# Optimization experiments

Measured on AMD Instinct MI355X. Metric: run time of the kernel, lower is better.

## Reference

```python
import jax, jax.numpy as jnp
import numpy as np
from jax.scipy.linalg import expm

D_LOGIC = 128
D_MEM = 16
SO_DIM = D_MEM * (D_MEM - 1) // 2  # 120


def _linear_init(key, fan_in, shape):
    bound = 1.0 / np.sqrt(fan_in)
    return jax.random.uniform(key, shape, jnp.float32, -bound, bound)


def setup_inputs() -> dict:
    key = jax.random.key(0)
    ks = jax.random.split(key, 14)
    B, S = 4, 128
    return {
        "x_logic": jax.random.normal(ks[0], (B, S, D_LOGIC), jnp.float32),
        "x_memory": jax.random.normal(ks[1], (B, S, D_MEM), jnp.float32),
        # W_Q / W_K
        "Wq": _linear_init(ks[2], D_LOGIC, (D_LOGIC, D_LOGIC)),
        "bq": _linear_init(ks[3], D_LOGIC, (D_LOGIC,)),
        "Wk": _linear_init(ks[4], D_LOGIC, (D_LOGIC, D_LOGIC)),
        "bk": _linear_init(ks[5], D_LOGIC, (D_LOGIC,)),
        # gamma_net: Linear(d_logic, 2*d_logic) -> Tanh -> Linear(2*d_logic, so_dim)
        "W1": _linear_init(ks[6], D_LOGIC, (2 * D_LOGIC, D_LOGIC)),
        "b1": _linear_init(ks[7], D_LOGIC, (2 * D_LOGIC,)),
        "W2": _linear_init(ks[8], 2 * D_LOGIC, (SO_DIM, 2 * D_LOGIC)),
        "b2": _linear_init(ks[9], 2 * D_LOGIC, (SO_DIM,)),
        # out_proj: Linear(d_memory, d_memory)
        "Wo": _linear_init(ks[10], D_MEM, (D_MEM, D_MEM)),
        "bo": _linear_init(ks[11], D_MEM, (D_MEM,)),
    }


def reference(x_logic, x_memory, Wq, bq, Wk, bk, W1, b1, W2, b2, Wo, bo):
    B, S, d_logic = x_logic.shape
    dm = x_memory.shape[-1]

    # attention over logic stream
    Q = x_logic @ Wq.T + bq
    K = x_logic @ Wk.T + bk
    attn = jax.nn.softmax(
        jnp.einsum("bjd,bid->bji", Q, K) / jnp.sqrt(jnp.float32(d_logic)), axis=-1
    )  # [B, S(j), S(i)]

    # per-pair Lie-algebra params: delta[b,j,i] = x_logic[b,j] - x_logic[b,i]
    delta = x_logic[:, :, None, :] - x_logic[:, None, :, :]  # [B,S,S,d_logic]
    h = jnp.tanh(delta @ W1.T + b1)
    lie = h @ W2.T + b2  # [B,S,S,so_dim]

    # scatter into skew-symmetric matrices [B,S,S,dm,dm]
    r, c = np.triu_indices(dm, k=1)
    skew = jnp.zeros((B, S, S, dm, dm), x_logic.dtype)
    skew = skew.at[..., r, c].set(lie)
    skew = skew.at[..., c, r].set(-lie)

    # Lie-group exponential -> orthogonal transport matrices
    T_all = expm(skew)  # [B,S,S,dm,dm]

    # transported[b,j,i,:] = T[b,j,i] @ x_memory[b,i]
    transported = jnp.einsum("bjide,bie->bjid", T_all, x_memory)

    # attention-weighted aggregation over i
    settled = jnp.einsum("bji,bjid->bjd", attn, transported)  # [B,S,dm]

    out = settled @ Wo.T + bo
    return out, T_all
```

## Files before the change

kernel.cpp:

```cpp
#include <hip/hip_runtime.h>
#include <hip/hip_fp16.h>

#define S_LEN 128
#define DLOG  128
#define DMEM  16
#define SO    120
#define HDIM  256

typedef _Float16 v8h __attribute__((ext_vector_type(8)));
typedef __fp16 v2hf __attribute__((ext_vector_type(2)));
typedef float v4f __attribute__((ext_vector_type(4)));

union PkU { v2hf h; unsigned u; };
union V8U { v8h v; int u[4]; };

__device__ __forceinline__ v8h splat8(float x) {
  _Float16 h = (_Float16)x;
  v8h v = {h, h, h, h, h, h, h, h};
  return v;
}

__global__ __launch_bounds__(512) void qku_kernel(
    const float* __restrict__ xl, const float* __restrict__ Wq,
    const float* __restrict__ bq, const float* __restrict__ Wk,
    const float* __restrict__ bk, const float* __restrict__ W1,
    float* __restrict__ Q, float* __restrict__ K, float* __restrict__ u) {
  int bj = blockIdx.x, t = threadIdx.x;
  int lane = t & 63, wu = t >> 6;
  int half = lane >> 5, l5 = lane & 31;
  float4 xv = *(const float4*)(xl + bj * 128 + 4 * l5);
  int seg = wu >> 1;
  const float* wb;
  if (seg == 0) wb = Wq;
  else if (seg == 1) wb = Wk - 128 * 128;
  else wb = W1 - 256 * 128;
  #pragma unroll 4
  for (int step = 0; step < 32; ++step) {
    int ro = wu * 64 + 2 * step + half;
    float4 wv = *(const float4*)(wb + ro * 128 + 4 * l5);
    float v = fmaf(wv.x, xv.x, fmaf(wv.y, xv.y, fmaf(wv.z, xv.z, wv.w * xv.w)));
    v += __shfl_xor(v, 1, 64);
    v += __shfl_xor(v, 2, 64);
    v += __shfl_xor(v, 4, 64);
    v += __shfl_xor(v, 8, 64);
    v += __shfl_xor(v, 16, 64);
    if (l5 == 0) {
      if (seg == 0) Q[bj * 128 + ro] = v + bq[ro];
      else if (seg == 1) K[bj * 128 + (ro - 128)] = v + bk[ro - 128];
      else u[bj * 256 + (ro - 256)] = v;
    }
  }
}

__global__ __launch_bounds__(256) void attn_h_kernel(
    const float* __restrict__ Q, const float* __restrict__ K,
    float* __restrict__ attn, const float* __restrict__ u,
    const float* __restrict__ b1, _Float16* __restrict__ hG) {
  int t = threadIdx.x;
  if (blockIdx.x < 256) {
    int sub = t >> 7, t128 = t & 127;
    int bj = blockIdx.x * 2 + sub, b = bj >> 7;
    int lane = t & 63, wu = (t >> 6) & 1;
    int half = lane >> 5, l5 = lane & 31;
    __shared__ float sc[2][128];
    __shared__ float red[2][128];
    float4 qv = *(const float4*)(Q + bj * 128 + 4 * l5);
    #pragma unroll 4
    for (int step = 0; step < 32; ++step) {
      int ro = wu * 64 + 2 * step + half;
      float4 kv = *(const float4*)(K + (size_t)(b * 128 + ro) * 128 + 4 * l5);
      float v = fmaf(kv.x, qv.x, fmaf(kv.y, qv.y, fmaf(kv.z, qv.z, kv.w * qv.w)));
      v += __shfl_xor(v, 1, 64);
      v += __shfl_xor(v, 2, 64);
      v += __shfl_xor(v, 4, 64);
      v += __shfl_xor(v, 8, 64);
      v += __shfl_xor(v, 16, 64);
      if (l5 == 0) sc[sub][ro] = v * 0.08838834764831845f;
    }
    __syncthreads();
    int i = t128;
    float s = sc[sub][i];
    red[sub][i] = s;
    __syncthreads();
    for (int off = 64; off; off >>= 1) {
      if (i < off) red[sub][i] = fmaxf(red[sub][i], red[sub][i + off]);
      __syncthreads();
    }
    float m = red[sub][0];
    __syncthreads();
    float e = expf(s - m);
    red[sub][i] = e;
    __syncthreads();
    for (int off = 64; off; off >>= 1) {
      if (i < off) red[sub][i] += red[sub][i + off];
      __syncthreads();
    }
    attn[(size_t)bj * 128 + i] = e / red[sub][0];
    return;
  }
  int tid = (blockIdx.x - 256) * 256 + t;
  #pragma unroll
  for (int g = 0; g < 4; ++g) {
    int unit = tid + g * 524288;
    int p = unit >> 5;
    int o0 = (unit & 31) * 8;
    int bj = p >> 7;
    int b = bj >> 7;
    int i = p & 127;
    const float* uj = u + bj * 256 + o0;
    const float* ui = u + (size_t)(b * 128 + i) * 256 + o0;
    const float* bb = b1 + o0;
    float4 j0 = *(const float4*)uj, j1 = *(const float4*)(uj + 4);
    float4 i0 = *(const float4*)ui, i1 = *(const float4*)(ui + 4);
    float4 c0 = *(const float4*)bb, c1 = *(const float4*)(bb + 4);
    float xv[8] = {j0.x - i0.x + c0.x, j0.y - i0.y + c0.y,
                   j0.z - i0.z + c0.z, j0.w - i0.w + c0.w,
                   j1.x - i1.x + c1.x, j1.y - i1.y + c1.y,
                   j1.z - i1.z + c1.z, j1.w - i1.w + c1.w};
    float rv[8];
    #pragma unroll
    for (int k = 0; k < 8; ++k) {
      float x = xv[k];
      float ax = fabsf(x);
      float e = __expf(-2.f * ax);
      float r = __fdividef(1.f - e, 1.f + e);
      rv[k] = copysignf(r, x);
    }
    V8U out;
    #pragma unroll
    for (int k = 0; k < 4; ++k) {
      PkU pu;
      pu.h = __builtin_amdgcn_cvt_pkrtz(rv[2 * k], rv[2 * k + 1]);
      out.u[k] = (int)pu.u;
    }
    *(v8h*)(hG + (size_t)p * 512 + o0) = out.v;
  }
}

__global__ __launch_bounds__(512) void lie_kernel(
    const float* __restrict__ W2g, const float* __restrict__ b2g,
    float* __restrict__ Tg) {
  __shared__ _Float16 w2t[128 * 136];
  int t = threadIdx.x, lane = t & 63;
  int wu = __builtin_amdgcn_readfirstlane(t >> 6);
  int pbase = blockIdx.x * 128 + wu * 16;
  int nn = lane & 15, q = lane >> 4;
  const _Float16* hf = (const _Float16*)Tg;

  for (int idx = t; idx < 1088; idx += 512) w2t[16320 + idx] = (_Float16)0.f;

  v4f acc[8];
  #pragma unroll
  for (int tt = 0; tt < 8; ++tt) acc[tt] = (v4f){0.f, 0.f, 0.f, 0.f};

  const _Float16* hrow = hf + (size_t)(pbase + nn) * 512;
  for (int khalf = 0; khalf < 2; ++khalf) {
    __syncthreads();
    for (int idx = t; idx < 3840; idx += 512) {
      int row = idx >> 5, c4 = (idx & 31) * 4;
      float4 v = *(const float4*)(W2g + row * 256 + khalf * 128 + c4);
      PkU a, b;
      a.h = __builtin_amdgcn_cvt_pkrtz(v.x, v.y);
      b.h = __builtin_amdgcn_cvt_pkrtz(v.z, v.w);
      uint2 pk = {a.u, b.u};
      *(uint2*)(w2t + row * 136 + c4) = pk;
    }
    __syncthreads();
    #pragma unroll
    for (int ks = 0; ks < 4; ++ks) {
      v8h ah = *(const v8h*)(hrow + khalf * 128 + ks * 32 + 8 * q);
      #pragma unroll
      for (int tt = 0; tt < 8; ++tt) {
        const v8h bf = *(const v8h*)(w2t + (16 * tt + nn) * 136 + ks * 32 + 8 * q);
        acc[tt] = __builtin_amdgcn_mfma_f32_16x16x32_f16(ah, bf, acc[tt], 0, 0, 0);
      }
    }
  }

  int rc0[8], rc1[8];
  float bbv[8];
  bool val[8];
  #pragma unroll
  for (int tt = 0; tt < 8; ++tt) {
    int n16 = 16 * tt + nn;
    val[tt] = (n16 < 120);
    float fr_ = floorf((31.0f - sqrtf(961.0f - 8.0f * (float)n16)) * 0.5f);
    int r = (int)fr_;
    int Sr = 15 * r - ((r * (r - 1)) >> 1);
    int c = n16 - Sr + r + 1;
    rc0[tt] = r * 16 + c;
    rc1[tt] = c * 16 + r;
    bbv[tt] = val[tt] ? b2g[n16] : 0.f;
  }

  _Float16* hw = (_Float16*)Tg;
  _Float16* aSt = w2t;
  for (int pass = 0; pass < 2; ++pass) {
    __syncthreads();
    #pragma unroll
    for (int reg = 0; reg < 4; ++reg) {
      int pidx = 4 * q + reg;
      if ((pidx >> 3) == pass) {
        _Float16* ab = aSt + (wu * 8 + (pidx & 7)) * 256;
        #pragma unroll
        for (int tt = 0; tt < 8; ++tt) {
          if (val[tt]) {
            _Float16 hv = (_Float16)(acc[tt][reg] + bbv[tt]);
            ab[rc0[tt]] = hv;
            ab[rc1[tt]] = -hv;
          }
        }
        ab[nn * 17] = (_Float16)0.f;
      }
    }
    __syncthreads();
    #pragma unroll
    for (int k = 0; k < 4; ++k) {
      int unit = t + k * 512;
      int lp = unit >> 5, off = (unit & 31) * 8;
      int g = blockIdx.x * 128 + (lp >> 3) * 16 + pass * 8 + (lp & 7);
      *(v8h*)(hw + (size_t)g * 512 + 256 + off) = *(const v8h*)(aSt + lp * 256 + off);
    }
  }
}

__device__ __forceinline__ void split8(const float* x, v8h& hi, v8h& lo) {
  union U { v8h v; v2hf p[4]; } H, L;
  #pragma unroll
  for (int i = 0; i < 4; ++i) {
    float a = x[2 * i], b = x[2 * i + 1];
    v2hf h = __builtin_amdgcn_cvt_pkrtz(a, b);
    float ra = (float)h[0], rb = (float)h[1];
    v2hf l = __builtin_amdgcn_cvt_pkrtz(a - ra, b - rb);
    H.p[i] = h;
    L.p[i] = l;
  }
  hi = H.v;
  lo = L.v;
}

__global__ __launch_bounds__(256) void expm_kernel(
    float* __restrict__ Tg, const float* __restrict__ attn,
    const float* __restrict__ xm, float* __restrict__ part) {
  __shared__ float ErB_all[4][1280];
  __shared__ float sred[4][16];
  int t = threadIdx.x, lane = t & 63;
  int wu = __builtin_amdgcn_readfirstlane(t >> 6);
  int pbase = blockIdx.x * 16 + wu * 4;
  int nn = lane & 15, q = lane >> 4, b8 = (q & 1) * 8;
  float* ErW = ErB_all[wu];
  const _Float16* hf = (const _Float16*)Tg;

  int idxA = ((2 * (q & 1)) * 16 + nn) * 4;
  int idxB = idxA + 64;

  float scv[4];
  int sv[4];
  V8U Apk[4];
  v4f Af[4];
  #pragma unroll
  for (int j = 0; j < 4; ++j) {
    size_t p = (size_t)(pbase + j);
    const _Float16* Ap = hf + p * 512 + 256;
    v8h rowh = *(const v8h*)(Ap + nn * 16 + b8);
    float s2 = 0.f;
    #pragma unroll
    for (int k = 0; k < 8; ++k) {
      float xf = (float)rowh[k];
      s2 = fmaf(xf, xf, s2);
    }
    #pragma unroll
    for (int off = 1; off < 64; off <<= 1) s2 += __shfl_xor(s2, off, 64);
    float bound = 0.5f * sqrtf(s2);
    int bb = __float_as_int(bound);
    int s = ((bb >> 23) & 255) - 126;
    s = min(max(s, 0), 12);
    sv[j] = __builtin_amdgcn_readfirstlane(s);
    scv[j] = __int_as_float((127 - sv[j]) << 23);
    v8h sch = splat8(scv[j]);
    V8U ap;
    ap.v = rowh * sch;
    #pragma unroll
    for (int i = 0; i < 4; ++i) Apk[j].u[i] = ap.u[i];
    #pragma unroll
    for (int reg = 0; reg < 4; ++reg)
      Af[j][reg] = (float)Ap[(4 * q + reg) * 16 + nn] * scv[j];
  }

  V8U IC1, IC2;
  #pragma unroll
  for (int i = 0; i < 4; ++i) {
    float d0 = (b8 + 2 * i == nn) ? 1.f : 0.f;
    float d1 = (b8 + 2 * i + 1 == nn) ? 1.f : 0.f;
    PkU u1, u2;
    u1.h = __builtin_amdgcn_cvt_pkrtz(10.666667f * d0, 10.666667f * d1);
    u2.h = __builtin_amdgcn_cvt_pkrtz(2.1333333f * d0, 2.1333333f * d1);
    IC1.u[i] = (int)u1.u;
    IC2.u[i] = (int)u2.u;
  }
  v8h k1a = splat8(7.9365079e-4f);
  v8h k1b = splat8(0.17777778f);
  v8h k2a = splat8(8.8183422e-5f);
  v8h k2b = splat8(2.5396825e-2f);
  v4f z4 = {0.f, 0.f, 0.f, 0.f};

  v4f cB[4];
  #pragma unroll
  for (int j = 0; j < 4; ++j) {
    V8U bfa;
    #pragma unroll
    for (int i = 0; i < 4; ++i) bfa.u[i] = Apk[j].u[i] ^ 0x80008000;
    cB[j] = __builtin_amdgcn_mfma_f32_16x16x32_f16(Apk[j].v, bfa.v, z4, 0, 0, 0);
  }

  V8U fB[4];
  #pragma unroll
  for (int j = 0; j < 4; ++j) {
    PkU u0, u1;
    u0.h = __builtin_amdgcn_cvt_pkrtz(cB[j][0], cB[j][1]);
    u1.h = __builtin_amdgcn_cvt_pkrtz(cB[j][2], cB[j][3]);
    fB[j].u[0] = __builtin_amdgcn_ds_bpermute(idxA, (int)u0.u);
    fB[j].u[1] = __builtin_amdgcn_ds_bpermute(idxA, (int)u1.u);
    fB[j].u[2] = __builtin_amdgcn_ds_bpermute(idxB, (int)u0.u);
    fB[j].u[3] = __builtin_amdgcn_ds_bpermute(idxB, (int)u1.u);
  }

  V8U fB2[4];
  #pragma unroll
  for (int j = 0; j < 4; ++j) {
    v4f c = __builtin_amdgcn_mfma_f32_16x16x32_f16(fB[j].v, fB[j].v, z4, 0, 0, 0);
    PkU u0, u1;
    u0.h = __builtin_amdgcn_cvt_pkrtz(c[0], c[1]);
    u1.h = __builtin_amdgcn_cvt_pkrtz(c[2], c[3]);
    fB2[j].u[0] = __builtin_amdgcn_ds_bpermute(idxA, (int)u0.u);
    fB2[j].u[1] = __builtin_amdgcn_ds_bpermute(idxA, (int)u1.u);
    fB2[j].u[2] = __builtin_amdgcn_ds_bpermute(idxB, (int)u0.u);
    fB2[j].u[3] = __builtin_amdgcn_ds_bpermute(idxB, (int)u1.u);
  }

  v4f E[4];
  #pragma unroll
  for (int j = 0; j < 4; ++j) {
    V8U M1, M2;
    M1.v = fB2[j].v * k1a + (fB[j].v * k1b + IC1.v);
    M2.v = fB2[j].v * k2a + (fB[j].v * k2b + IC2.v);
    v4f c3m = __builtin_amdgcn_mfma_f32_16x16x32_f16(M1.v, fB2[j].v, z4, 0, 0, 0);
    v4f c4m = __builtin_amdgcn_mfma_f32_16x16x32_f16(M2.v, fB2[j].v, z4, 0, 0, 0);
    v4f Cc, Qc;
    #pragma unroll
    for (int reg = 0; reg < 4; ++reg) {
      float dg = (4 * q + reg == nn) ? 1.f : 0.f;
      Cc[reg] = fmaf(c3m[reg], 2.44140625e-4f,
                     fmaf(cB[j][reg], 0.25f, dg + Af[j][reg]));
      Qc[reg] = fmaf(c4m[reg], 2.44140625e-4f, cB[j][reg] * 0.083333333f);
    }
    PkU u0, u1;
    u0.h = __builtin_amdgcn_cvt_pkrtz(Qc[0], Qc[1]);
    u1.h = __builtin_amdgcn_cvt_pkrtz(Qc[2], Qc[3]);
    V8U fQ;
    fQ.u[0] = __builtin_amdgcn_ds_bpermute(idxA, (int)u0.u);
    fQ.u[1] = __builtin_amdgcn_ds_bpermute(idxA, (int)u1.u);
    fQ.u[2] = __builtin_amdgcn_ds_bpermute(idxB, (int)u0.u);
    fQ.u[3] = __builtin_amdgcn_ds_bpermute(idxB, (int)u1.u);
    v4f c5 = __builtin_amdgcn_mfma_f32_16x16x32_f16(Apk[j].v, fQ.v, z4, 0, 0, 0);
    E[j] = Cc + c5 * 0.5f;
  }

  int smax = max(max(sv[0], sv[1]), max(sv[2], sv[3]));
  for (int it = 0; it < smax; ++it) {
    #pragma unroll
    for (int j = 0; j < 4; ++j) {
      if (it < sv[j]) {
        float* Erp = ErW + j * 320;
        PkU u0, u1;
        u0.h = __builtin_amdgcn_cvt_pkrtz(E[j][0], E[j][1]);
        u1.h = __builtin_amdgcn_cvt_pkrtz(E[j][2], E[j][3]);
        V8U bfe;
        bfe.u[0] = __builtin_amdgcn_ds_bpermute(idxA, (int)u0.u);
        bfe.u[1] = __builtin_amdgcn_ds_bpermute(idxA, (int)u1.u);
        bfe.u[2] = __builtin_amdgcn_ds_bpermute(idxB, (int)u0.u);
        bfe.u[3] = __builtin_amdgcn_ds_bpermute(idxB, (int)u1.u);
        #pragma unroll
        for (int reg = 0; reg < 4; ++reg)
          Erp[(4 * q + reg) * 20 + nn] = E[j][reg];
        asm volatile("s_waitcnt lgkmcnt(0)" ::: "memory");
        float4 a0 = *(const float4*)(Erp + nn * 20 + b8);
        float4 a1 = *(const float4*)(Erp + nn * 20 + b8 + 4);
        float xa[8] = {a0.x, a0.y, a0.z, a0.w, a1.x, a1.y, a1.z, a1.w};
        v8h ahi, alo;
        split8(xa, ahi, alo);
        v8h Ecat = (q < 2) ? ahi : alo;
        v4f z = {0.f, 0.f, 0.f, 0.f};
        E[j] = __builtin_amdgcn_mfma_f32_16x16x32_f16(Ecat, bfe.v, z, 0, 0, 0);
      }
    }
  }

  float pacc[4] = {0.f, 0.f, 0.f, 0.f};
  #pragma unroll
  for (int j = 0; j < 4; ++j) {
    int p = pbase + j;
    float* dst = Tg + (size_t)p * 256;
    #pragma unroll
    for (int reg = 0; reg < 4; ++reg)
      dst[(4 * q + reg) * 16 + nn] = E[j][reg];
    int b = p >> 14, i = p & 127;
    float xv = xm[((b << 7) + i) * 16 + nn];
    float aw = attn[(size_t)p] * xv;
    #pragma unroll
    for (int reg = 0; reg < 4; ++reg)
      pacc[reg] = fmaf(aw, E[j][reg], pacc[reg]);
  }
  #pragma unroll
  for (int reg = 0; reg < 4; ++reg) {
    #pragma unroll
    for (int off = 1; off < 16; off <<= 1)
      pacc[reg] += __shfl_xor(pacc[reg], off, 64);
  }
  if (nn == 0) {
    #pragma unroll
    for (int reg = 0; reg < 4; ++reg) sred[wu][4 * q + reg] = pacc[reg];
  }
  __syncthreads();
  if (t < 16)
    part[(size_t)blockIdx.x * 16 + t] =
        sred[0][t] + sred[1][t] + sred[2][t] + sred[3][t];
}

__global__ __launch_bounds__(64) void settle_fin_kernel(
    const float* __restrict__ part, const float* __restrict__ Wo,
    const float* __restrict__ bo, float* __restrict__ outp) {
  int bj = blockIdx.x, t = threadIdx.x;
  int r = t & 15, e0 = t >> 4;
  const float* pb = part + (size_t)bj * 128;
  float s = pb[e0 * 16 + r] + pb[(e0 + 4) * 16 + r];
  __shared__ float sf[64];
  sf[t] = s;
  __syncthreads();
  if (t < 16) sf[t] = sf[t] + sf[16 + t] + sf[32 + t] + sf[48 + t];
  __syncthreads();
  if (t < 16) {
    float o = bo[t];
    const float* wr = Wo + t * 16;
    #pragma unroll
    for (int c = 0; c < 16; ++c) o = fmaf(wr[c], sf[c], o);
    outp[bj * 16 + t] = o;
  }
}

extern "C" void kernel_launch(void* const* d_in, const int* in_sizes, int n_in,
                              void* d_out, int out_size, void* d_ws,
                              size_t ws_size, hipStream_t stream) {
  const float* xl = (const float*)d_in[0];
  const float* xm = (const float*)d_in[1];
  const float* Wq = (const float*)d_in[2];
  const float* bq = (const float*)d_in[3];
  const float* Wk = (const float*)d_in[4];
  const float* bk = (const float*)d_in[5];
  const float* W1 = (const float*)d_in[6];
  const float* b1 = (const float*)d_in[7];
  const float* W2 = (const float*)d_in[8];
  const float* b2 = (const float*)d_in[9];
  const float* Wo = (const float*)d_in[10];
  const float* bo = (const float*)d_in[11];
  float* outp = (float*)d_out;
  float* Tg = outp + 8192;
  float* wsf = (float*)d_ws;
  float* Q = wsf;
  float* K = wsf + 65536;
  float* attn = wsf + 131072;
  float* u = wsf + 196608;
  float* part = wsf + 196608;

  hipLaunchKernelGGL(qku_kernel, dim3(512), dim3(512), 0, stream, xl, Wq, bq, Wk, bk, W1, Q, K, u);
  hipLaunchKernelGGL(attn_h_kernel, dim3(2304), dim3(256), 0, stream, Q, K, attn, u, b1, (_Float16*)Tg);
  hipLaunchKernelGGL(lie_kernel, dim3(512), dim3(512), 0, stream, W2, b2, Tg);
  hipLaunchKernelGGL(expm_kernel, dim3(4096), dim3(256), 0, stream, Tg, attn, xm, part);
  hipLaunchKernelGGL(settle_fin_kernel, dim3(512), dim3(64), 0, stream, part, Wo, bo, outp);
}
```

Baseline: 186.3 us.

## Fuse tanh hidden-layer computation into lie_kernel MFMA operand load

```diff
diff --git a/kernel.cpp b/kernel.cpp
--- a/kernel.cpp
+++ b/kernel.cpp
@@ -52,127 +52,114 @@
   }
 }
 
-__global__ __launch_bounds__(256) void attn_h_kernel(
+__global__ __launch_bounds__(256) void attn_kernel(
     const float* __restrict__ Q, const float* __restrict__ K,
-    float* __restrict__ attn, const float* __restrict__ u,
-    const float* __restrict__ b1, _Float16* __restrict__ hG) {
+    float* __restrict__ attn) {
   int t = threadIdx.x;
-  if (blockIdx.x < 256) {
-    int sub = t >> 7, t128 = t & 127;
-    int bj = blockIdx.x * 2 + sub, b = bj >> 7;
-    int lane = t & 63, wu = (t >> 6) & 1;
-    int half = lane >> 5, l5 = lane & 31;
-    __shared__ float sc[2][128];
-    __shared__ float red[2][128];
-    float4 qv = *(const float4*)(Q + bj * 128 + 4 * l5);
-    #pragma unroll 4
-    for (int step = 0; step < 32; ++step) {
-      int ro = wu * 64 + 2 * step + half;
-      float4 kv = *(const float4*)(K + (size_t)(b * 128 + ro) * 128 + 4 * l5);
-      float v = fmaf(kv.x, qv.x, fmaf(kv.y, qv.y, fmaf(kv.z, qv.z, kv.w * qv.w)));
-      v += __shfl_xor(v, 1, 64);
-      v += __shfl_xor(v, 2, 64);
-      v += __shfl_xor(v, 4, 64);
-      v += __shfl_xor(v, 8, 64);
-      v += __shfl_xor(v, 16, 64);
-      if (l5 == 0) sc[sub][ro] = v * 0.08838834764831845f;
-    }
-    __syncthreads();
-    int i = t128;
-    float s = sc[sub][i];
-    red[sub][i] = s;
-    __syncthreads();
-    for (int off = 64; off; off >>= 1) {
-      if (i < off) red[sub][i] = fmaxf(red[sub][i], red[sub][i + off]);
-      __syncthreads();
-    }
-    float m = red[sub][0];
-    __syncthreads();
-    float e = expf(s - m);
-    red[sub][i] = e;
-    __syncthreads();
-    for (int off = 64; off; off >>= 1) {
-      if (i < off) red[sub][i] += red[sub][i + off];
-      __syncthreads();
-    }
-    attn[(size_t)bj * 128 + i] = e / red[sub][0];
-    return;
-  }
-  int tid = (blockIdx.x - 256) * 256 + t;
-  #pragma unroll
-  for (int g = 0; g < 4; ++g) {
-    int unit = tid + g * 524288;
-    int p = unit >> 5;
-    int o0 = (unit & 31) * 8;
-    int bj = p >> 7;
-    int b = bj >> 7;
-    int i = p & 127;
-    const float* uj = u + bj * 256 + o0;
-    const float* ui = u + (size_t)(b * 128 + i) * 256 + o0;
-    const float* bb = b1 + o0;
-    float4 j0 = *(const float4*)uj, j1 = *(const float4*)(uj + 4);
-    float4 i0 = *(const float4*)ui, i1 = *(const float4*)(ui + 4);
-    float4 c0 = *(const float4*)bb, c1 = *(const float4*)(bb + 4);
-    float xv[8] = {j0.x - i0.x + c0.x, j0.y - i0.y + c0.y,
-                   j0.z - i0.z + c0.z, j0.w - i0.w + c0.w,
-                   j1.x - i1.x + c1.x, j1.y - i1.y + c1.y,
-                   j1.z - i1.z + c1.z, j1.w - i1.w + c1.w};
-    float rv[8];
-    #pragma unroll
-    for (int k = 0; k < 8; ++k) {
-      float x = xv[k];
-      float ax = fabsf(x);
-      float e = __expf(-2.f * ax);
-      float r = __fdividef(1.f - e, 1.f + e);
-      rv[k] = copysignf(r, x);
-    }
-    V8U out;
-    #pragma unroll
-    for (int k = 0; k < 4; ++k) {
-      PkU pu;
-      pu.h = __builtin_amdgcn_cvt_pkrtz(rv[2 * k], rv[2 * k + 1]);
-      out.u[k] = (int)pu.u;
-    }
-    *(v8h*)(hG + (size_t)p * 512 + o0) = out.v;
-  }
+  int sub = t >> 7, t128 = t & 127;
+  int bj = blockIdx.x * 2 + sub, b = bj >> 7;
+  int lane = t & 63, wu = (t >> 6) & 1;
+  int half = lane >> 5, l5 = lane & 31;
+  __shared__ float sc[2][128];
+  __shared__ float red[2][128];
+  float4 qv = *(const float4*)(Q + bj * 128 + 4 * l5);
+  #pragma unroll 4
+  for (int step = 0; step < 32; ++step) {
+    int ro = wu * 64 + 2 * step + half;
+    float4 kv = *(const float4*)(K + (size_t)(b * 128 + ro) * 128 + 4 * l5);
+    float v = fmaf(kv.x, qv.x, fmaf(kv.y, qv.y, fmaf(kv.z, qv.z, kv.w * qv.w)));
+    v += __shfl_xor(v, 1, 64);
+    v += __shfl_xor(v, 2, 64);
+    v += __shfl_xor(v, 4, 64);
+    v += __shfl_xor(v, 8, 64);
+    v += __shfl_xor(v, 16, 64);
+    if (l5 == 0) sc[sub][ro] = v * 0.08838834764831845f;
+  }
+  __syncthreads();
+  int i = t128;
+  float s = sc[sub][i];
+  red[sub][i] = s;
+  __syncthreads();
+  for (int off = 64; off; off >>= 1) {
+    if (i < off) red[sub][i] = fmaxf(red[sub][i], red[sub][i + off]);
+    __syncthreads();
+  }
+  float m = red[sub][0];
+  __syncthreads();
+  float e = expf(s - m);
+  red[sub][i] = e;
+  __syncthreads();
+  for (int off = 64; off; off >>= 1) {
+    if (i < off) red[sub][i] += red[sub][i + off];
+    __syncthreads();
+  }
+  attn[(size_t)bj * 128 + i] = e / red[sub][0];
 }
 
 __global__ __launch_bounds__(512) void lie_kernel(
     const float* __restrict__ W2g, const float* __restrict__ b2g,
+    const float* __restrict__ ug, const float* __restrict__ b1g,
     float* __restrict__ Tg) {
   __shared__ _Float16 w2t[128 * 136];
+  __shared__ float ujb[256];
   int t = threadIdx.x, lane = t & 63;
   int wu = __builtin_amdgcn_readfirstlane(t >> 6);
-  int pbase = blockIdx.x * 128 + wu * 16;
+  int bj = blockIdx.x;
+  int b = bj >> 7;
   int nn = lane & 15, q = lane >> 4;
-  const _Float16* hf = (const _Float16*)Tg;
-
+  int irow = wu * 16 + nn;
+
+  if (t < 256) ujb[t] = ug[bj * 256 + t] + b1g[t];
   for (int idx = t; idx < 1088; idx += 512) w2t[16320 + idx] = (_Float16)0.f;
 
   v4f acc[8];
   #pragma unroll
   for (int tt = 0; tt < 8; ++tt) acc[tt] = (v4f){0.f, 0.f, 0.f, 0.f};
 
-  const _Float16* hrow = hf + (size_t)(pbase + nn) * 512;
+  const float* uib = ug + (size_t)(b * 128 + irow) * 256;
+
   for (int khalf = 0; khalf < 2; ++khalf) {
     __syncthreads();
     for (int idx = t; idx < 3840; idx += 512) {
       int row = idx >> 5, c4 = (idx & 31) * 4;
       float4 v = *(const float4*)(W2g + row * 256 + khalf * 128 + c4);
-      PkU a, b;
+      PkU a, b2;
       a.h = __builtin_amdgcn_cvt_pkrtz(v.x, v.y);
-      b.h = __builtin_amdgcn_cvt_pkrtz(v.z, v.w);
-      uint2 pk = {a.u, b.u};
+      b2.h = __builtin_amdgcn_cvt_pkrtz(v.z, v.w);
+      uint2 pk = {a.u, b2.u};
       *(uint2*)(w2t + row * 136 + c4) = pk;
     }
     __syncthreads();
     #pragma unroll
     for (int ks = 0; ks < 4; ++ks) {
-      v8h ah = *(const v8h*)(hrow + khalf * 128 + ks * 32 + 8 * q);
+      int k0 = khalf * 128 + ks * 32 + 8 * q;
+      float4 ui0 = *(const float4*)(uib + k0);
+      float4 ui1 = *(const float4*)(uib + k0 + 4);
+      float4 uj0 = *(const float4*)(ujb + k0);
+      float4 uj1 = *(const float4*)(ujb + k0 + 4);
+      float xv[8] = {uj0.x - ui0.x, uj0.y - ui0.y, uj0.z - ui0.z,
+                     uj0.w - ui0.w, uj1.x - ui1.x, uj1.y - ui1.y,
+                     uj1.z - ui1.z, uj1.w - ui1.w};
+      float rv[8];
+      #pragma unroll
+      for (int k = 0; k < 8; ++k) {
+        float x = xv[k];
+        float ax = fabsf(x);
+        float e = __expf(-2.f * ax);
+        float r = __fdividef(1.f - e, 1.f + e);
+        rv[k] = copysignf(r, x);
+      }
+      V8U ah;
+      #pragma unroll
+      for (int k = 0; k < 4; ++k) {
+        PkU pu;
+        pu.h = __builtin_amdgcn_cvt_pkrtz(rv[2 * k], rv[2 * k + 1]);
+        ah.u[k] = (int)pu.u;
+      }
       #pragma unroll
       for (int tt = 0; tt < 8; ++tt) {
         const v8h bf = *(const v8h*)(w2t + (16 * tt + nn) * 136 + ks * 32 + 8 * q);
-        acc[tt] = __builtin_amdgcn_mfma_f32_16x16x32_f16(ah, bf, acc[tt], 0, 0, 0);
+        acc[tt] = __builtin_amdgcn_mfma_f32_16x16x32_f16(ah.v, bf, acc[tt], 0, 0, 0);
       }
     }
   }
@@ -218,7 +205,7 @@
     for (int k = 0; k < 4; ++k) {
       int unit = t + k * 512;
       int lp = unit >> 5, off = (unit & 31) * 8;
-      int g = blockIdx.x * 128 + (lp >> 3) * 16 + pass * 8 + (lp & 7);
+      int g = bj * 128 + (lp >> 3) * 16 + pass * 8 + (lp & 7);
       *(v8h*)(hw + (size_t)g * 512 + 256 + off) = *(const v8h*)(aSt + lp * 256 + off);
     }
   }
@@ -473,8 +460,8 @@
   float* part = wsf + 196608;
 
   hipLaunchKernelGGL(qku_kernel, dim3(512), dim3(512), 0, stream, xl, Wq, bq, Wk, bk, W1, Q, K, u);
-  hipLaunchKernelGGL(attn_h_kernel, dim3(2304), dim3(256), 0, stream, Q, K, attn, u, b1, (_Float16*)Tg);
-  hipLaunchKernelGGL(lie_kernel, dim3(512), dim3(512), 0, stream, W2, b2, Tg);
+  hipLaunchKernelGGL(attn_kernel, dim3(256), dim3(256), 0, stream, Q, K, attn);
+  hipLaunchKernelGGL(lie_kernel, dim3(512), dim3(512), 0, stream, W2, b2, u, b1, Tg);
   hipLaunchKernelGGL(expm_kernel, dim3(4096), dim3(256), 0, stream, Tg, attn, xm, part);
   hipLaunchKernelGGL(settle_fin_kernel, dim3(512), dim3(64), 0, stream, part, Wo, bo, outp);
 }
```

New measurement: 190.1 us. 1.02x slower.
